# Optimization experiments

Hardware: AMD Instinct MI355X
Metric: run time of the kernel (lower is better)

The kernel has to match this reference:

```python
import jax, jax.numpy as jnp
import numpy as np


def setup_inputs() -> dict:
    key = jax.random.key(0)
    k1, k2 = jax.random.split(key)
    x = jax.random.normal(k1, (8, 32, 252, 252), dtype=jnp.float32)
    weight = jax.random.normal(k2, (32, 32, 5, 5), dtype=jnp.float32)
    return {"x": x, "weight": weight}


def reference(x, weight):
    # FFT-based conv2d, mathematically identical to the torch module but with
    # the batch-invariant weight FFT hoisted out of the batch dimension.
    k = weight.shape[-1]
    p = k // 2
    # reflect padding (matches F.pad mode='reflect')
    xp = jnp.pad(x, ((0, 0), (0, 0), (p, p), (p, p)), mode="reflect")
    H, W = xp.shape[-2], xp.shape[-1]
    # embed kernel in top-left of a full-size zero canvas, then circular roll
    # by (-k)//2 (Python floor division, as in the original torch code)
    wp = jnp.zeros((weight.shape[0], weight.shape[1], H, W), dtype=x.dtype)
    wp = wp.at[:, :, :k, :k].set(weight)
    shift = (-k) // 2  # e.g. k=5 -> -3, matching torch.roll(shifts=(-k//2,...))
    wp = jnp.roll(wp, shift=(shift, shift), axis=(-2, -1))
    x_fft = jnp.fft.fft2(xp)          # [B, I, H, W] complex
    w_fft = jnp.fft.fft2(wp)          # [O, I, H, W] complex (no batch copy)
    out_fft = jnp.einsum("bihw,oihw->bohw", x_fft, w_fft)
    out = jnp.fft.ifft2(out_fft).real
    return out[:, :, p:-p, p:-p]
```

## Files before the change

kernel.cpp:

```cpp
#include <hip/hip_runtime.h>
#include <hip/hip_bf16.h>

typedef __attribute__((ext_vector_type(8))) short bf16x8;
typedef __attribute__((ext_vector_type(4))) float f32x4;

#define HW_   252
#define PLANE 63504
#define NCH   32
#define WS_NEED (25600u * 2u)

__device__ __forceinline__ unsigned short f2bf(float f) {
    unsigned u = __builtin_bit_cast(unsigned, f);
    u += 0x7FFFu + ((u >> 16) & 1u);
    return (unsigned short)(u >> 16);
}

__device__ __forceinline__ int padmap(int p) {
    int t = (p & 255) - 2;
    t = t < 0 ? -t : t;
    return t > 251 ? 502 - t : t;
}

__global__ void pack_w_kernel(const float* __restrict__ w, unsigned short* __restrict__ wp) {
    int e = blockIdx.x * 256 + threadIdx.x;
    if (e >= 25600) return;
    int ci = e & 31;
    int o  = (e >> 5) & 31;
    int t  = e >> 10;
    int da = t / 5, db = t - da * 5;
    wp[e] = f2bf(w[((o * 32 + ci) * 5 + (4 - da)) * 5 + (4 - db)]);
}

__global__ __launch_bounds__(256, 4) void conv_fused_v8(
    const float* __restrict__ x,
    const unsigned short* __restrict__ wp,
    float* __restrict__ out)
{
    __shared__ unsigned short xl[32 * 20 * 32];

    const int tid  = threadIdx.x;
    const int orig = blockIdx.x;
    const int b    = orig & 7;
    const int idx  = orig >> 3;
    const int rt   = idx >> 4;
    const int ct   = idx & 15;
    const int i0 = rt * 28, j0 = ct * 16;

    float v[10][8];
    {
        const float* xb = x + (size_t)b * NCH * PLANE;
        #pragma unroll
        for (int it = 0; it < 10; ++it) {
            int task = it * 256 + tid;
            int g    = task & 3;
            int pc   = task >> 2;
            int pr   = pc / 20;
            int col  = pc - pr * 20;
            const float* src = xb + (size_t)(g * 8) * PLANE
                                  + (size_t)padmap(i0 + 1 + pr) * HW_
                                  + padmap(j0 + 1 + col);
            #pragma unroll
            for (int q = 0; q < 8; ++q)
                v[it][q] = src[q * PLANE];
        }
    }
    #pragma unroll
    for (int it = 0; it < 10; ++it) {
        int task = it * 256 + tid;
        unsigned short pk[8];
        #pragma unroll
        for (int q = 0; q < 8; ++q)
            pk[q] = __builtin_bit_cast(unsigned short,
                        __float2bfloat16(v[it][q]));
        *reinterpret_cast<uint4*>(reinterpret_cast<char*>(xl) + task * 16)
            = *reinterpret_cast<const uint4*>(pk);
    }
    __syncthreads();

    const int lane = tid & 63;
    const int wid  = tid >> 6;
    const int lm   = lane & 15;
    const int lg   = lane >> 4;
    const int rowb = wid * 7;

    const char* xlb = reinterpret_cast<const char*>(xl);
    const char* wb  = reinterpret_cast<const char*>(wp);
    const int afix  = (lm << 6) + (lg << 4);

    f32x4 acc[7][2];
    #pragma unroll
    for (int r = 0; r < 7; ++r) {
        acc[r][0] = (f32x4){0.f, 0.f, 0.f, 0.f};
        acc[r][1] = (f32x4){0.f, 0.f, 0.f, 0.f};
    }

    #pragma unroll
    for (int db = 0; db < 5; ++db) {
        bf16x8 a[5][2];
        #pragma unroll
        for (int da = 0; da < 5; ++da) {
            const char* ap = wb + ((da * 5 + db) << 11) + afix;
            a[da][0] = *reinterpret_cast<const bf16x8*>(ap);
            a[da][1] = *reinterpret_cast<const bf16x8*>(ap + 1024);
        }

        #pragma unroll
        for (int l = 0; l < 11; ++l) {
            bf16x8 bf = *reinterpret_cast<const bf16x8*>(
                xlb + (rowb + l) * 1280 + ((lm + db) << 6) + (lg << 4));
            #pragma unroll
            for (int da = 0; da < 5; ++da) {
                const int r = l - da;
                if (r >= 0 && r < 7) {
                    acc[r][0] = __builtin_amdgcn_mfma_f32_16x16x32_bf16(
                        bf, a[da][0], acc[r][0], 0, 0, 0);
                    acc[r][1] = __builtin_amdgcn_mfma_f32_16x16x32_bf16(
                        bf, a[da][1], acc[r][1], 0, 0, 0);
                }
            }
        }
    }

    const int jq = j0 + (lg << 2);
    if (jq + 3 < HW_) {
        #pragma unroll
        for (int r = 0; r < 7; ++r) {
            const int i = i0 + rowb + r;
            #pragma unroll
            for (int mt = 0; mt < 2; ++mt) {
                float* dst = out + ((size_t)(b * NCH + mt * 16 + lm)) * PLANE
                           + (size_t)i * HW_ + jq;
                *reinterpret_cast<float4*>(dst) =
                    *reinterpret_cast<const float4*>(&acc[r][mt]);
            }
        }
    }
}

__global__ __launch_bounds__(256) void conv_mfma_fb(
    const float* __restrict__ x,
    const float* __restrict__ w_raw,
    float* __restrict__ out)
{
    __shared__ unsigned short xl[12800];
    __shared__ unsigned short wl[25600];
    __shared__ int rmap[20], cmap[20];

    const int tid = threadIdx.x;
    const int bid = blockIdx.x;
    const int b  = bid >> 8;
    const int rt = (bid >> 4) & 15;
    const int ct = bid & 15;
    const int i0 = rt * 16, j0 = ct * 16;

    if (tid < 40) {
        int k    = tid < 20 ? tid : tid - 20;
        int base = tid < 20 ? i0  : j0;
        int r = (base + 1 + k) & 255;
        int t = r - 2;
        int m = t < 0 ? -t : (t > 251 ? 502 - t : t);
        if (tid < 20) rmap[k] = m; else cmap[k] = m;
    }
    for (int e = tid; e < 25600; e += 256) {
        int o   = e / 800;
        int rem = e - o * 800;
        int ci  = rem / 25;
        int kd  = rem - ci * 25;
        wl[(24 - kd) * 1024 + o * 32 + ci] = f2bf(w_raw[e]);
    }
    __syncthreads();

    for (int task = tid; task < 1600; task += 256) {
        int col = task % 20;
        int g   = (task / 20) & 3;
        int row = task / 80;
        const float* src = x + (size_t)(b * NCH + g * 8) * PLANE
                             + (size_t)rmap[row] * HW_ + cmap[col];
        unsigned short pk[8];
        #pragma unroll
        for (int q = 0; q < 8; ++q) pk[q] = f2bf(src[q * PLANE]);
        int off = ((row * 20 + col) << 6) + ((g ^ (col & 3)) << 4);
        *reinterpret_cast<uint4*>(reinterpret_cast<char*>(xl) + off)
            = *reinterpret_cast<const uint4*>(pk);
    }
    __syncthreads();

    const int lane  = tid & 63;
    const int wid   = tid >> 6;
    const int lm    = lane & 15;
    const int lg    = lane >> 4;
    const int rbase = wid * 4;

    f32x4 acc[4][2];
    #pragma unroll
    for (int rr = 0; rr < 4; ++rr) {
        acc[rr][0] = (f32x4){0.f, 0.f, 0.f, 0.f};
        acc[rr][1] = (f32x4){0.f, 0.f, 0.f, 0.f};
    }

    const char* wbase = (const char*)wl;
    const int afix = (lm << 6) + (lg << 4);
    const char* xlb = reinterpret_cast<const char*>(xl);

    #pragma unroll
    for (int da = 0; da < 5; ++da) {
        #pragma unroll
        for (int db = 0; db < 5; ++db) {
            const int t = da * 5 + db;
            bf16x8 a0 = *reinterpret_cast<const bf16x8*>(wbase + (t << 11) + afix);
            bf16x8 a1 = *reinterpret_cast<const bf16x8*>(wbase + (t << 11) + 1024 + afix);
            const int col  = lm + db;
            const int coff = (col << 6) + ((lg ^ (col & 3)) << 4);
            #pragma unroll
            for (int rr = 0; rr < 4; ++rr) {
                const int row = rbase + rr + da;
                bf16x8 bf = *reinterpret_cast<const bf16x8*>(xlb + row * 1280 + coff);
                acc[rr][0] = __builtin_amdgcn_mfma_f32_16x16x32_bf16(a0, bf, acc[rr][0], 0, 0, 0);
                acc[rr][1] = __builtin_amdgcn_mfma_f32_16x16x32_bf16(a1, bf, acc[rr][1], 0, 0, 0);
            }
        }
    }

    const int j = j0 + lm;
    #pragma unroll
    for (int rr = 0; rr < 4; ++rr) {
        const int i = i0 + rbase + rr;
        if (i < HW_ && j < HW_) {
            size_t rowoff = (size_t)(b * NCH) * PLANE + (size_t)i * HW_ + j;
            #pragma unroll
            for (int mt = 0; mt < 2; ++mt)
                #pragma unroll
                for (int q = 0; q < 4; ++q) {
                    int o = mt * 16 + lg * 4 + q;
                    out[rowoff + (size_t)o * PLANE] = acc[rr][mt][q];
                }
        }
    }
}

extern "C" void kernel_launch(void* const* d_in, const int* in_sizes, int n_in,
                              void* d_out, int out_size, void* d_ws, size_t ws_size,
                              hipStream_t stream) {
    const float* x = (const float*)d_in[0];
    const float* w = (const float*)d_in[1];
    float* out = (float*)d_out;

    if (ws_size >= WS_NEED) {
        unsigned short* wp = (unsigned short*)d_ws;
        hipLaunchKernelGGL(pack_w_kernel, dim3(100), dim3(256), 0, stream, w, wp);
        hipLaunchKernelGGL(conv_fused_v8, dim3(1152), dim3(256), 0, stream,
                           x, (const unsigned short*)wp, out);
    } else {
        hipLaunchKernelGGL(conv_mfma_fb, dim3(2048), dim3(256), 0, stream, x, w, out);
    }
}
```

Baseline: 47.90 us.

## Stage input tile via global_load_lds double-buffered DMA with overlapped bf16 conversion

```diff
diff --git a/kernel.cpp b/kernel.cpp
--- a/kernel.cpp
+++ b/kernel.cpp
@@ -31,12 +31,14 @@
     wp[e] = f2bf(w[((o * 32 + ci) * 5 + (4 - da)) * 5 + (4 - db)]);
 }
 
-__global__ __launch_bounds__(256, 4) void conv_fused_v8(
+__global__ __launch_bounds__(256, 2) void conv_fused_v9(
     const float* __restrict__ x,
     const unsigned short* __restrict__ wp,
     float* __restrict__ out)
 {
     __shared__ unsigned short xl[32 * 20 * 32];
+    __shared__ float fbA[8 * 20 * 32];
+    __shared__ float fbB[8 * 20 * 32];
 
     const int tid  = threadIdx.x;
     const int orig = blockIdx.x;
@@ -46,42 +48,65 @@
     const int ct   = idx & 15;
     const int i0 = rt * 28, j0 = ct * 16;
 
-    float v[10][8];
-    {
-        const float* xb = x + (size_t)b * NCH * PLANE;
-        #pragma unroll
-        for (int it = 0; it < 10; ++it) {
-            int task = it * 256 + tid;
-            int g    = task & 3;
-            int pc   = task >> 2;
-            int pr   = pc / 20;
-            int col  = pc - pr * 20;
-            const float* src = xb + (size_t)(g * 8) * PLANE
-                                  + (size_t)padmap(i0 + 1 + pr) * HW_
-                                  + padmap(j0 + 1 + col);
-            #pragma unroll
-            for (int q = 0; q < 8; ++q)
-                v[it][q] = src[q * PLANE];
-        }
-    }
-    #pragma unroll
-    for (int it = 0; it < 10; ++it) {
-        int task = it * 256 + tid;
-        unsigned short pk[8];
-        #pragma unroll
-        for (int q = 0; q < 8; ++q)
-            pk[q] = __builtin_bit_cast(unsigned short,
-                        __float2bfloat16(v[it][q]));
-        *reinterpret_cast<uint4*>(reinterpret_cast<char*>(xl) + task * 16)
-            = *reinterpret_cast<const uint4*>(pk);
-    }
+    const int wv   = tid >> 6;
+    const int half = (tid >> 5) & 1;
+    const bool interior = (j0 != 0) && (j0 != 240);
+
+    const float* pb = x + (size_t)b * NCH * PLANE + (size_t)(tid & 31) * PLANE;
+
+    auto DMA = [&](int c, float* fb) {
+        const int rb = i0 + 1 + c * 8 + wv * 2;
+        const int mrLo = padmap(rb);
+        const int mrHi = padmap(rb + 1);
+        #pragma unroll
+        for (int i = 0; i < 20; ++i) {
+            const int mr = (i >= 10) ? mrHi : mrLo;
+            const int ca = (2 * i) % 20;
+            int mcA, mcB;
+            if (interior) { mcA = j0 - 1 + ca; mcB = j0 + ca; }
+            else { mcA = padmap(j0 + 1 + ca); mcB = padmap(j0 + 2 + ca); }
+            const int mc = half ? mcB : mcA;
+            const float* src = pb + (size_t)mr * HW_ + mc;
+            __builtin_amdgcn_global_load_lds(
+                (const __attribute__((address_space(1))) void*)src,
+                (__attribute__((address_space(3))) void*)(fb + wv * 1280 + i * 64),
+                4, 0, 0);
+        }
+    };
+
+    auto CONVERT = [&](int c, const float* fb) {
+        #pragma unroll
+        for (int it = 0; it < 3; ++it) {
+            int t = it * 256 + tid;
+            if (t < 640) {
+                int g  = t & 3;
+                int cc = t >> 2;
+                const char* rbp = reinterpret_cast<const char*>(fb) + cc * 128 + g * 32;
+                float4 f0 = *reinterpret_cast<const float4*>(rbp);
+                float4 f1 = *reinterpret_cast<const float4*>(rbp + 16);
+                unsigned short pk[8] = {
+                    f2bf(f0.x), f2bf(f0.y), f2bf(f0.z), f2bf(f0.w),
+                    f2bf(f1.x), f2bf(f1.y), f2bf(f1.z), f2bf(f1.w)};
+                *reinterpret_cast<uint4*>(reinterpret_cast<char*>(xl)
+                    + ((size_t)(c * 160 + cc) * 4 + g) * 16)
+                    = *reinterpret_cast<const uint4*>(pk);
+            }
+        }
+    };
+
+    DMA(0, fbA);
     __syncthreads();
+    #pragma unroll
+    for (int c = 0; c < 4; ++c) {
+        if (c < 3) DMA(c + 1, (c & 1) ? fbA : fbB);
+        CONVERT(c, (c & 1) ? fbB : fbA);
+        __syncthreads();
+    }
 
     const int lane = tid & 63;
-    const int wid  = tid >> 6;
     const int lm   = lane & 15;
     const int lg   = lane >> 4;
-    const int rowb = wid * 7;
+    const int rowb = wv * 7;
 
     const char* xlb = reinterpret_cast<const char*>(xl);
     const char* wb  = reinterpret_cast<const char*>(wp);
@@ -248,7 +273,7 @@
     if (ws_size >= WS_NEED) {
         unsigned short* wp = (unsigned short*)d_ws;
         hipLaunchKernelGGL(pack_w_kernel, dim3(100), dim3(256), 0, stream, w, wp);
-        hipLaunchKernelGGL(conv_fused_v8, dim3(1152), dim3(256), 0, stream,
+        hipLaunchKernelGGL(conv_fused_v9, dim3(1152), dim3(256), 0, stream,
                            x, (const unsigned short*)wp, out);
     } else {
         hipLaunchKernelGGL(conv_mfma_fb, dim3(2048), dim3(256), 0, stream, x, w, out);
```

New measurement: 84.18 us. 75.8% more time.
